# Kernel tuning notes

Measured on AMD Instinct MI355X. Metric: run time of the kernel, lower is better.

The kernel has to match this reference:

```python
import jax, jax.numpy as jnp
import numpy as np
from functools import partial


def _lstm_layer(x, W_ih, b_ih, W_hh, b_hh):
    # x: [B, T, D]; W_ih: [4H, D]; W_hh: [4H, H]
    B = x.shape[0]
    H = W_hh.shape[1]
    # Batch the input projection over all timesteps (one big GEMM).
    xg = jnp.einsum('btd,gd->btg', x, W_ih) + b_ih + b_hh  # [B, T, 4H]
    h0 = jnp.zeros((B, H), dtype=x.dtype)
    c0 = jnp.zeros((B, H), dtype=x.dtype)

    def step(carry, xg_t):
        h, c = carry
        gates = xg_t + h @ W_hh.T  # [B, 4H]
        i, f, g, o = jnp.split(gates, 4, axis=-1)
        i = jax.nn.sigmoid(i)
        f = jax.nn.sigmoid(f)
        g = jnp.tanh(g)
        o = jax.nn.sigmoid(o)
        c = f * c + i * g
        h = o * jnp.tanh(c)
        return (h, c), h

    (h_T, c_T), ys = jax.lax.scan(step, (h0, c0), jnp.swapaxes(xg, 0, 1))
    return jnp.swapaxes(ys, 0, 1), h_T, c_T  # [B, T, H], [B, H], [B, H]


def setup_inputs() -> dict:
    key = jax.random.key(0)
    ks = jax.random.split(key, 8)
    B, T, D, H = 64, 512, 1024, 1024
    s = 1.0 / np.sqrt(H)
    return {
        'X': jax.random.normal(ks[0], (B, T, D), jnp.float32),
        'W_ih_0': jax.random.normal(ks[1], (4 * H, D), jnp.float32) * s,
        'b_ih_0': jnp.zeros((4 * H,), jnp.float32),
        'W_hh_0': jax.random.normal(ks[2], (4 * H, H), jnp.float32) * s,
        'b_hh_0': jnp.zeros((4 * H,), jnp.float32),
        'W_ih_1': jax.random.normal(ks[3], (4 * H, H), jnp.float32) * s,
        'b_ih_1': jnp.zeros((4 * H,), jnp.float32),
        'W_hh_1': jax.random.normal(ks[4], (4 * H, H), jnp.float32) * s,
        'b_hh_1': jnp.zeros((4 * H,), jnp.float32),
    }


def reference(X, W_ih_0, b_ih_0, W_hh_0, b_hh_0, W_ih_1, b_ih_1, W_hh_1, b_hh_1):
    out0, h0, c0 = _lstm_layer(X, W_ih_0, b_ih_0, W_hh_0, b_hh_0)
    out1, h1, c1 = _lstm_layer(out0, W_ih_1, b_ih_1, W_hh_1, b_hh_1)
    h_n = jnp.stack([h0, h1], axis=0)  # [num_layers, B, H]
    c_n = jnp.stack([c0, c1], axis=0)
    return out1, (h_n, c_n)
```

## Files before the change

### kernel.cpp

```cpp
#include <hip/hip_runtime.h>
#include <type_traits>

typedef _Float16 half8 __attribute__((ext_vector_type(8)));
typedef _Float16 half4v __attribute__((ext_vector_type(4)));
typedef float f32x4 __attribute__((ext_vector_type(4)));
typedef unsigned long long u64;

struct U128 { u64 a, b; };

#define B_ 64
#define T_ 512
#define H_ 1024
#define G_ 4096
#define K_ 1024
#define MPROJ (B_ * T_)

__global__ void k_f32_to_f16(const float* __restrict__ s, _Float16* __restrict__ d, int n4) {
  int i = blockIdx.x * 256 + threadIdx.x;
  if (i < n4) {
    float4 v = ((const float4*)s)[i];
    half4v o;
    o[0] = (_Float16)v.x; o[1] = (_Float16)v.y; o[2] = (_Float16)v.z; o[3] = (_Float16)v.w;
    ((half4v*)d)[i] = o;
  }
}

__global__ void k_bias(const float* __restrict__ bi0, const float* __restrict__ bh0,
                       const float* __restrict__ bi1, const float* __restrict__ bh1,
                       float* __restrict__ o0, float* __restrict__ o1) {
  int i = blockIdx.x * 256 + threadIdx.x;
  if (i < G_) { o0[i] = bi0[i] + bh0[i]; o1[i] = bi1[i] + bh1[i]; }
}

__global__ void k_zero(uint4* __restrict__ p, int n) {
  int i = blockIdx.x * 256 + threadIdx.x;
  if (i < n) p[i] = make_uint4(0u, 0u, 0u, 0u);
}

template <typename AT>
__global__ __launch_bounds__(256, 2) void k_proj(const AT* __restrict__ A,
                                                 const _Float16* __restrict__ Bw,
                                                 const float* __restrict__ bias,
                                                 _Float16* __restrict__ C) {
  const int NBN = G_ / 128;
  int bm = blockIdx.x / NBN;
  int bn = blockIdx.x % NBN;
  __shared__ __align__(16) _Float16 As[128 * 40];
  __shared__ __align__(16) _Float16 Bs[128 * 40];
  int tid = threadIdx.x;
  int lane = tid & 63, wave = tid >> 6;
  int wm = (wave >> 1) * 64, wn = (wave & 1) * 64;
  int quad = lane >> 4, l16 = lane & 15;
  f32x4 acc[4][4] = {};
  int r = tid >> 1;
  int hc = (tid & 1) * 16;
  const AT* aRow = A + (size_t)(bm * 128 + r) * K_ + hc;
  const _Float16* bRow = Bw + (size_t)(bn * 128 + r) * K_ + hc;
  _Float16* aDst = As + r * 40 + hc;
  _Float16* bDst = Bs + r * 40 + hc;

  for (int kt = 0; kt < K_ / 32; ++kt) {
    if constexpr (std::is_same<AT, float>::value) {
      float tmp[16];
      *(float4*)(tmp + 0)  = *(const float4*)(aRow + 0);
      *(float4*)(tmp + 4)  = *(const float4*)(aRow + 4);
      *(float4*)(tmp + 8)  = *(const float4*)(aRow + 8);
      *(float4*)(tmp + 12) = *(const float4*)(aRow + 12);
      half8 h0, h1;
#pragma unroll
      for (int e = 0; e < 8; ++e) { h0[e] = (_Float16)tmp[e]; h1[e] = (_Float16)tmp[e + 8]; }
      *(half8*)(aDst) = h0;
      *(half8*)(aDst + 8) = h1;
    } else {
      *(half8*)(aDst) = *(const half8*)(aRow);
      *(half8*)(aDst + 8) = *(const half8*)(aRow + 8);
    }
    *(half8*)(bDst) = *(const half8*)(bRow);
    *(half8*)(bDst + 8) = *(const half8*)(bRow + 8);
    __syncthreads();
    half8 af[4], bf[4];
#pragma unroll
    for (int i = 0; i < 4; ++i) af[i] = *(const half8*)(As + (wm + i * 16 + l16) * 40 + quad * 8);
#pragma unroll
    for (int j = 0; j < 4; ++j) bf[j] = *(const half8*)(Bs + (wn + j * 16 + l16) * 40 + quad * 8);
#pragma unroll
    for (int i = 0; i < 4; ++i)
#pragma unroll
      for (int j = 0; j < 4; ++j)
        acc[i][j] = __builtin_amdgcn_mfma_f32_16x16x32_f16(af[i], bf[j], acc[i][j], 0, 0, 0);
    __syncthreads();
    aRow += 32;
    bRow += 32;
  }
#pragma unroll
  for (int j = 0; j < 4; ++j) {
    int n = bn * 128 + wn + j * 16 + l16;
    float bv = bias[n];
#pragma unroll
    for (int i = 0; i < 4; ++i) {
      size_t m0 = (size_t)(bm * 128 + wm + i * 16 + quad * 4);
#pragma unroll
      for (int rr = 0; rr < 4; ++rr)
        C[(m0 + rr) * G_ + n] = (_Float16)(acc[i][j][rr] + bv);
    }
  }
}

__global__ __launch_bounds__(512) void k_fused(
    const _Float16* __restrict__ xg,
    const _Float16* __restrict__ Whh0,
    const _Float16* __restrict__ Wih1,
    const _Float16* __restrict__ Whh1,
    const float* __restrict__ b1,
    _Float16* __restrict__ h0a, _Float16* __restrict__ h0b,
    _Float16* __restrict__ h1a, _Float16* __restrict__ h1b,
    unsigned int* cnt_base,
    float* __restrict__ out32,
    float* __restrict__ hn0, float* __restrict__ cn0,
    float* __restrict__ hn1, float* __restrict__ cn1) {
  int g = blockIdx.x & 3;
  int wid = blockIdx.x >> 2;
  int u0 = wid * 16;
  int b0 = g * 16;
  int tid = threadIdx.x;
  int lane = tid & 63, w = tid >> 6;
  int quad = lane >> 4, l16 = lane & 15;
  unsigned int* cnt = cnt_base + g * 16;

  __shared__ float part[8][8][16][18];
  __shared__ float red[8][16][18];
  __shared__ float cs[2][16][16];
  __shared__ __align__(16) _Float16 wi1_lds[2 * 16 * 1032];
  __shared__ int step_flag;
  ((float*)cs)[tid] = 0.f;
  if (tid == 0) step_flag = 0;

  for (int idx = tid; idx < 2 * 16 * (K_ / 8); idx += 512) {
    int gt2 = idx >> 11;
    int r = (idx >> 7) & 15;
    int c = idx & 127;
    half8 v = *(const half8*)(Wih1 + (size_t)((2 + gt2) * H_ + u0 + r) * K_ + c * 8);
    *(half8*)(wi1_lds + (gt2 * 16 + r) * 1032 + c * 8) = v;
  }

  int ks = w * 128;
  half8 wf0[4][4], wh1[4][4], wi1r[2][4];
#pragma unroll
  for (int gt = 0; gt < 4; ++gt)
#pragma unroll
    for (int kk = 0; kk < 4; ++kk) {
      wf0[gt][kk] = *(const half8*)(Whh0 + (size_t)(gt * H_ + u0 + l16) * K_ + ks + kk * 32 + quad * 8);
      wh1[gt][kk] = *(const half8*)(Whh1 + (size_t)(gt * H_ + u0 + l16) * K_ + ks + kk * 32 + quad * 8);
    }
#pragma unroll
  for (int gt = 0; gt < 2; ++gt)
#pragma unroll
    for (int kk = 0; kk < 4; ++kk)
      wi1r[gt][kk] = *(const half8*)(Wih1 + (size_t)(gt * H_ + u0 + l16) * K_ + ks + kk * 32 + quad * 8);

  int fm = (w & 3) * 4 + quad;
  float b1v[4] = {};
  if (w >= 4) {
#pragma unroll
    for (int gt = 0; gt < 4; ++gt) b1v[gt] = b1[gt * H_ + u0 + l16];
  }
  __syncthreads();

  for (int i = 0; i <= T_; ++i) {
    const _Float16* h0r = (i & 1) ? h0b : h0a;
    _Float16* h0w = (i & 1) ? h0a : h0b;
    const _Float16* h1r = (i & 1) ? h1b : h1a;
    _Float16* h1w = (i & 1) ? h1a : h1b;

    float pxi = 0.f, pxf = 0.f, pxg = 0.f, pxo = 0.f;
    if (w < 4 && i < T_) {
      const _Float16* xr = xg + ((size_t)(b0 + fm) * T_ + i) * G_ + u0 + l16;
      pxi = (float)xr[0];
      pxf = (float)xr[H_];
      pxg = (float)xr[2 * H_];
      pxo = (float)xr[3 * H_];
    }

    half8 af0[4], af1[4];
#pragma unroll
    for (int kk = 0; kk < 4; ++kk) {
      const _Float16* hs = h0r + (size_t)(b0 + l16) * H_ + ks + kk * 32 + quad * 8;
      u64 qlo = __hip_atomic_load((const u64*)hs, __ATOMIC_RELAXED, __HIP_MEMORY_SCOPE_AGENT);
      u64 qhi = __hip_atomic_load(((const u64*)hs) + 1, __ATOMIC_RELAXED, __HIP_MEMORY_SCOPE_AGENT);
      U128 u; u.a = qlo; u.b = qhi;
      af0[kk] = __builtin_bit_cast(half8, u);
    }
#pragma unroll
    for (int kk = 0; kk < 4; ++kk) {
      const _Float16* hs = h1r + (size_t)(b0 + l16) * H_ + ks + kk * 32 + quad * 8;
      u64 qlo = __hip_atomic_load((const u64*)hs, __ATOMIC_RELAXED, __HIP_MEMORY_SCOPE_AGENT);
      u64 qhi = __hip_atomic_load(((const u64*)hs) + 1, __ATOMIC_RELAXED, __HIP_MEMORY_SCOPE_AGENT);
      U128 u; u.a = qlo; u.b = qhi;
      af1[kk] = __builtin_bit_cast(half8, u);
    }

    {
      f32x4 acc[4] = {};
#pragma unroll
      for (int kk = 0; kk < 4; ++kk)
#pragma unroll
        for (int gt = 0; gt < 4; ++gt)
          acc[gt] = __builtin_amdgcn_mfma_f32_16x16x32_f16(af0[kk], wf0[gt][kk], acc[gt], 0, 0, 0);
#pragma unroll
      for (int gt = 0; gt < 4; ++gt)
#pragma unroll
        for (int rr = 0; rr < 4; ++rr)
          part[w][gt][quad * 4 + rr][l16] = acc[gt][rr];
    }
    {
      f32x4 bcc[4] = {};
#pragma unroll
      for (int kk = 0; kk < 4; ++kk) {
        bcc[0] = __builtin_amdgcn_mfma_f32_16x16x32_f16(af0[kk], wi1r[0][kk], bcc[0], 0, 0, 0);
        bcc[1] = __builtin_amdgcn_mfma_f32_16x16x32_f16(af0[kk], wi1r[1][kk], bcc[1], 0, 0, 0);
        half8 w2 = *(const half8*)(wi1_lds + (0 * 16 + l16) * 1032 + ks + kk * 32 + quad * 8);
        bcc[2] = __builtin_amdgcn_mfma_f32_16x16x32_f16(af0[kk], w2, bcc[2], 0, 0, 0);
        half8 w3 = *(const half8*)(wi1_lds + (1 * 16 + l16) * 1032 + ks + kk * 32 + quad * 8);
        bcc[3] = __builtin_amdgcn_mfma_f32_16x16x32_f16(af0[kk], w3, bcc[3], 0, 0, 0);
      }
#pragma unroll
      for (int kk = 0; kk < 4; ++kk)
#pragma unroll
        for (int gt = 0; gt < 4; ++gt)
          bcc[gt] = __builtin_amdgcn_mfma_f32_16x16x32_f16(af1[kk], wh1[gt][kk], bcc[gt], 0, 0, 0);
#pragma unroll
      for (int gt = 0; gt < 4; ++gt)
#pragma unroll
        for (int rr = 0; rr < 4; ++rr)
          part[w][4 + gt][quad * 4 + rr][l16] = bcc[gt][rr];
    }
    __syncthreads();

    {
#pragma unroll
      for (int rr = 0; rr < 4; ++rr) {
        int m = quad * 4 + rr;
        float sum = part[0][w][m][l16];
#pragma unroll
        for (int w2 = 1; w2 < 8; ++w2) sum += part[w2][w][m][l16];
        red[w][m][l16] = sum;
      }
    }
    __syncthreads();

    if (w < 4) {
      if (i < T_) {
        int m = fm, n = l16;
        float iv = red[0][m][n] + pxi;
        float fv = red[1][m][n] + pxf;
        float gv = red[2][m][n] + pxg;
        float ov = red[3][m][n] + pxo;
        float si = 1.f / (1.f + __expf(-iv));
        float sf = 1.f / (1.f + __expf(-fv));
        float so = 1.f / (1.f + __expf(-ov));
        float ag = fabsf(gv), eg = __expf(-2.f * ag);
        float tg = (1.f - eg) / (1.f + eg);
        tg = (gv < 0.f) ? -tg : tg;
        float c = sf * cs[0][m][n] + si * tg;
        cs[0][m][n] = c;
        float ac = fabsf(c), ec = __expf(-2.f * ac);
        float th = (1.f - ec) / (1.f + ec);
        th = (c < 0.f) ? -th : th;
        float h = so * th;
        unsigned short hu = __builtin_bit_cast(unsigned short, (_Float16)h);
        unsigned other = __shfl_xor((unsigned)hu, 1, 64);
        if ((l16 & 1) == 0) {
          unsigned packed = (unsigned)hu | (other << 16);
          __hip_atomic_store((unsigned*)(h0w + (size_t)(b0 + m) * H_ + u0 + l16), packed,
                             __ATOMIC_RELAXED, __HIP_MEMORY_SCOPE_AGENT);
        }
        if (i == T_ - 1) {
          hn0[(size_t)(b0 + m) * H_ + u0 + n] = h;
          cn0[(size_t)(b0 + m) * H_ + u0 + n] = c;
        }
      }
    } else {
      if (i >= 1) {
        int m = fm, n = l16;
        int j = i - 1;
        float iv = red[4][m][n] + b1v[0];
        float fv = red[5][m][n] + b1v[1];
        float gv = red[6][m][n] + b1v[2];
        float ov = red[7][m][n] + b1v[3];
        float si = 1.f / (1.f + __expf(-iv));
        float sf = 1.f / (1.f + __expf(-fv));
        float so = 1.f / (1.f + __expf(-ov));
        float ag = fabsf(gv), eg = __expf(-2.f * ag);
        float tg = (1.f - eg) / (1.f + eg);
        tg = (gv < 0.f) ? -tg : tg;
        float c = sf * cs[1][m][n] + si * tg;
        cs[1][m][n] = c;
        float ac = fabsf(c), ec = __expf(-2.f * ac);
        float th = (1.f - ec) / (1.f + ec);
        th = (c < 0.f) ? -th : th;
        float h = so * th;
        unsigned short hu = __builtin_bit_cast(unsigned short, (_Float16)h);
        unsigned other = __shfl_xor((unsigned)hu, 1, 64);
        if ((l16 & 1) == 0) {
          unsigned packed = (unsigned)hu | (other << 16);
          __hip_atomic_store((unsigned*)(h1w + (size_t)(b0 + m) * H_ + u0 + l16), packed,
                             __ATOMIC_RELAXED, __HIP_MEMORY_SCOPE_AGENT);
        }
        out32[((size_t)(b0 + m) * T_ + j) * H_ + u0 + n] = h;
        if (j == T_ - 1) {
          hn1[(size_t)(b0 + m) * H_ + u0 + n] = h;
          cn1[(size_t)(b0 + m) * H_ + u0 + n] = c;
        }
      }
    }
    __syncthreads();

    if (i == T_) break;
    unsigned int tgt = 64u * (unsigned)(i + 1);
    if (w == 0) {
      if (lane == 0)
        __hip_atomic_fetch_add(cnt, 1u, __ATOMIC_RELAXED, __HIP_MEMORY_SCOPE_AGENT);
      while (__hip_atomic_load(cnt, __ATOMIC_RELAXED, __HIP_MEMORY_SCOPE_AGENT) < tgt)
        __builtin_amdgcn_s_sleep(1);
      asm volatile("" ::: "memory");
      if (lane == 0) __atomic_store_n(&step_flag, i + 1, __ATOMIC_RELEASE);
    } else {
      while (__atomic_load_n(&step_flag, __ATOMIC_ACQUIRE) < i + 1)
        __builtin_amdgcn_s_sleep(1);
    }
  }
}

extern "C" void kernel_launch(void* const* d_in, const int* in_sizes, int n_in,
                              void* d_out, int out_size, void* d_ws, size_t ws_size,
                              hipStream_t stream) {
  (void)in_sizes; (void)n_in; (void)out_size;
  const float* X    = (const float*)d_in[0];
  const float* Wih0 = (const float*)d_in[1];
  const float* bih0 = (const float*)d_in[2];
  const float* Whh0 = (const float*)d_in[3];
  const float* bhh0 = (const float*)d_in[4];
  const float* Wih1 = (const float*)d_in[5];
  const float* bih1 = (const float*)d_in[6];
  const float* Whh1 = (const float*)d_in[7];
  const float* bhh1 = (const float*)d_in[8];
  float* out = (float*)d_out;
  char* ws = (char*)d_ws;

  constexpr size_t SZW = (size_t)G_ * K_ * 2;
  constexpr size_t OFF_B0   = 4 * SZW;
  constexpr size_t OFF_B1   = OFF_B0 + 16384;
  constexpr size_t OFF_CNT  = OFF_B1 + 16384;
  constexpr size_t OFF_HBUF = OFF_CNT + 16384;
  constexpr size_t OFF_XG   = OFF_HBUF + 4 * 131072;
  constexpr size_t NEED     = OFF_XG + (size_t)MPROJ * G_ * 2;
  if (ws_size < NEED) return;

  _Float16* Wih0h = (_Float16*)(ws + 0 * SZW);
  _Float16* Whh0h = (_Float16*)(ws + 1 * SZW);
  _Float16* Wih1h = (_Float16*)(ws + 2 * SZW);
  _Float16* Whh1h = (_Float16*)(ws + 3 * SZW);
  float* b0s = (float*)(ws + OFF_B0);
  float* b1s = (float*)(ws + OFF_B1);
  unsigned int* cnts = (unsigned int*)(ws + OFF_CNT);
  _Float16* hb = (_Float16*)(ws + OFF_HBUF);
  _Float16* h0a = hb;
  _Float16* h0b = hb + 65536;
  _Float16* h1a = hb + 131072;
  _Float16* h1b = hb + 196608;
  _Float16* xgp = (_Float16*)(ws + OFF_XG);

  k_f32_to_f16<<<4096, 256, 0, stream>>>(Wih0, Wih0h, G_ * K_ / 4);
  k_f32_to_f16<<<4096, 256, 0, stream>>>(Whh0, Whh0h, G_ * K_ / 4);
  k_f32_to_f16<<<4096, 256, 0, stream>>>(Wih1, Wih1h, G_ * K_ / 4);
  k_f32_to_f16<<<4096, 256, 0, stream>>>(Whh1, Whh1h, G_ * K_ / 4);
  k_bias<<<16, 256, 0, stream>>>(bih0, bhh0, bih1, bhh1, b0s, b1s);
  k_zero<<<132, 256, 0, stream>>>((uint4*)(ws + OFF_CNT), (int)((16384 + 4 * 131072) / 16));

  const int projGrid = (MPROJ / 128) * (G_ / 128);
  k_proj<float><<<dim3(projGrid), dim3(256), 0, stream>>>(X, Wih0h, b0s, xgp);

  {
    const _Float16* a0 = xgp;
    const _Float16* a1 = Whh0h;
    const _Float16* a2 = Wih1h;
    const _Float16* a3 = Whh1h;
    const float* a4 = b1s;
    _Float16* a5 = h0a;
    _Float16* a6 = h0b;
    _Float16* a7 = h1a;
    _Float16* a8 = h1b;
    unsigned int* a9 = cnts;
    float* a10 = out;
    float* a11 = out + 33554432;
    float* a12 = out + 33554432 + 131072;
    float* a13 = out + 33554432 + 65536;
    float* a14 = out + 33554432 + 131072 + 65536;
    void* args[15] = {&a0, &a1, &a2, &a3, &a4, &a5, &a6, &a7,
                      &a8, &a9, &a10, &a11, &a12, &a13, &a14};
    hipLaunchCooperativeKernel((void*)k_fused, dim3(256), dim3(512), args, 0, stream);
  }
}
```

Measured before the change: 5.037 ms.

## Replace atomic counter barrier with per-block step flags and defer output stores

The shared per-group atomic counter barrier is replaced by one flag slot per block: each block stores its step number, and a polling wave reads all 64 flags of its group in a single load and waits until every one has reached the target. This removes contention from many blocks doing fetch_add on one address. The fp32 output store for layer 1 is also moved past the barrier signal so that global write no longer delays the flag publication. In exchange there is more polling traffic, and correctness relies on relaxed-ordering and visibility assumptions for the h buffers.

```diff
diff --git a/kernel.cpp b/kernel.cpp
--- a/kernel.cpp
+++ b/kernel.cpp
@@ -114,7 +114,7 @@
     const float* __restrict__ b1,
     _Float16* __restrict__ h0a, _Float16* __restrict__ h0b,
     _Float16* __restrict__ h1a, _Float16* __restrict__ h1b,
-    unsigned int* cnt_base,
+    unsigned int* flags,
     float* __restrict__ out32,
     float* __restrict__ hn0, float* __restrict__ cn0,
     float* __restrict__ hn1, float* __restrict__ cn1) {
@@ -125,7 +125,7 @@
   int tid = threadIdx.x;
   int lane = tid & 63, w = tid >> 6;
   int quad = lane >> 4, l16 = lane & 15;
-  unsigned int* cnt = cnt_base + g * 16;
+  unsigned int* gf = flags + (g << 7);
 
   __shared__ float part[8][8][16][18];
   __shared__ float red[8][16][18];
@@ -248,6 +248,8 @@
     }
     __syncthreads();
 
+    float ph = 0.f;
+    size_t poidx = 0;
     if (w < 4) {
       if (i < T_) {
         int m = fm, n = l16;
@@ -306,7 +308,8 @@
           __hip_atomic_store((unsigned*)(h1w + (size_t)(b0 + m) * H_ + u0 + l16), packed,
                              __ATOMIC_RELAXED, __HIP_MEMORY_SCOPE_AGENT);
         }
-        out32[((size_t)(b0 + m) * T_ + j) * H_ + u0 + n] = h;
+        ph = h;
+        poidx = ((size_t)(b0 + m) * T_ + j) * H_ + u0 + n;
         if (j == T_ - 1) {
           hn1[(size_t)(b0 + m) * H_ + u0 + n] = h;
           cn1[(size_t)(b0 + m) * H_ + u0 + n] = c;
@@ -315,18 +318,28 @@
     }
     __syncthreads();
 
-    if (i == T_) break;
-    unsigned int tgt = 64u * (unsigned)(i + 1);
+    if (i == T_) {
+      if (w >= 4) out32[poidx] = ph;
+      break;
+    }
+    if (w == 1 && lane == 0)
+      __hip_atomic_store(gf + wid, (unsigned)(i + 1),
+                         __ATOMIC_RELAXED, __HIP_MEMORY_SCOPE_AGENT);
+    if (w >= 4 && i >= 1) out32[poidx] = ph;
+
+    unsigned tgt = (unsigned)(i + 1);
     if (w == 0) {
-      if (lane == 0)
-        __hip_atomic_fetch_add(cnt, 1u, __ATOMIC_RELAXED, __HIP_MEMORY_SCOPE_AGENT);
-      while (__hip_atomic_load(cnt, __ATOMIC_RELAXED, __HIP_MEMORY_SCOPE_AGENT) < tgt)
+      for (;;) {
+        unsigned v = __hip_atomic_load(gf + lane, __ATOMIC_RELAXED, __HIP_MEMORY_SCOPE_AGENT);
+        if (__all(v >= tgt)) break;
+        __builtin_amdgcn_s_sleep(1);
+      }
+      asm volatile("" ::: "memory");
+      if (lane == 0) __atomic_store_n(&step_flag, (int)tgt, __ATOMIC_RELEASE);
+    } else {
+      while (__atomic_load_n(&step_flag, __ATOMIC_ACQUIRE) < (int)tgt)
         __builtin_amdgcn_s_sleep(1);
       asm volatile("" ::: "memory");
-      if (lane == 0) __atomic_store_n(&step_flag, i + 1, __ATOMIC_RELEASE);
-    } else {
-      while (__atomic_load_n(&step_flag, __ATOMIC_ACQUIRE) < i + 1)
-        __builtin_amdgcn_s_sleep(1);
     }
   }
 }
@@ -362,7 +375,7 @@
   _Float16* Whh1h = (_Float16*)(ws + 3 * SZW);
   float* b0s = (float*)(ws + OFF_B0);
   float* b1s = (float*)(ws + OFF_B1);
-  unsigned int* cnts = (unsigned int*)(ws + OFF_CNT);
+  unsigned int* flgs = (unsigned int*)(ws + OFF_CNT);
   _Float16* hb = (_Float16*)(ws + OFF_HBUF);
   _Float16* h0a = hb;
   _Float16* h0b = hb + 65536;
@@ -390,7 +403,7 @@
     _Float16* a6 = h0b;
     _Float16* a7 = h1a;
     _Float16* a8 = h1b;
-    unsigned int* a9 = cnts;
+    unsigned int* a9 = flgs;
     float* a10 = out;
     float* a11 = out + 33554432;
     float* a12 = out + 33554432 + 131072;
```

After: 4.954 ms. About the same (-1.6%).
